# Kernel tuning notes

Measured on AMD Instinct MI355X. Metric: run time of the kernel, lower is better.

The kernel has to match this reference:

```python
import jax, jax.numpy as jnp
import numpy as np

N, E, IN, H, L = 50000, 640000, 64, 128, 3
EPS_DIST = 1e-8
LN_EPS = 1e-5


def setup_inputs() -> dict:
    key = jax.random.key(0)
    ks = iter(jax.random.split(key, 64))

    def rn(shape, fan_in):
        return (jax.random.normal(next(ks), shape, jnp.float32) / np.sqrt(fan_in)).astype(jnp.float32)

    inp = {}
    inp['h'] = jax.random.normal(next(ks), (N, IN), jnp.float32)
    inp['x'] = jax.random.normal(next(ks), (N, 3), jnp.float32)
    inp['edge_index'] = jax.random.randint(next(ks), (2, E), 0, N, jnp.int64)
    # embedding_in: Linear(IN, H)
    inp['W_emb'] = rn((IN, H), IN); inp['b_emb'] = jnp.zeros((H,), jnp.float32)
    # per-layer EquivariantConv params, stacked over L
    inp['Wm1'] = rn((L, 2 * H + 1, H), 2 * H + 1); inp['bm1'] = jnp.zeros((L, H), jnp.float32)
    inp['Wm2'] = rn((L, H, H), H);                 inp['bm2'] = jnp.zeros((L, H), jnp.float32)
    inp['Wc1'] = rn((L, H, H), H);                 inp['bc1'] = jnp.zeros((L, H), jnp.float32)
    inp['Wc2'] = rn((L, H, 1), H)  # no bias
    inp['Wn1'] = rn((L, 2 * H, H), 2 * H);         inp['bn1'] = jnp.zeros((L, H), jnp.float32)
    inp['Wn2'] = rn((L, H, H), H);                 inp['bn2'] = jnp.zeros((L, H), jnp.float32)
    inp['ln_g'] = jnp.ones((L, H), jnp.float32);   inp['ln_b'] = jnp.zeros((L, H), jnp.float32)
    # epsilon head params
    inp['Wem1'] = rn((2 * H + 4, H), 2 * H + 4);   inp['bem1'] = jnp.zeros((H,), jnp.float32)
    inp['Wem2'] = rn((H, H), H);                   inp['bem2'] = jnp.zeros((H,), jnp.float32)
    inp['Wec1'] = rn((H, H), H);                   inp['bec1'] = jnp.zeros((H,), jnp.float32)
    inp['Wec2'] = rn((H, 3), H);                   inp['bec2'] = jnp.zeros((3,), jnp.float32)
    inp['Wh1'] = rn((H + 3, H), H + 3);            inp['bh1'] = jnp.zeros((H,), jnp.float32)
    inp['Wh2'] = rn((H, 3), H);                    inp['bh2'] = jnp.zeros((3,), jnp.float32)
    return inp


def _layernorm(v, g, b):
    mu = jnp.mean(v, axis=-1, keepdims=True)
    var = jnp.mean((v - mu) ** 2, axis=-1, keepdims=True)
    return (v - mu) * jax.lax.rsqrt(var + LN_EPS) * g + b


def reference(h, x, edge_index, W_emb, b_emb, Wm1, bm1, Wm2, bm2, Wc1, bc1, Wc2,
              Wn1, bn1, Wn2, bn2, ln_g, ln_b, Wem1, bem1, Wem2, bem2,
              Wec1, bec1, Wec2, bec2, Wh1, bh1, Wh2, bh2):
    row, col = edge_index[0], edge_index[1]
    n = x.shape[0]
    seg = lambda v: jax.ops.segment_sum(v, col, num_segments=n)
    in_degree = seg(jnp.ones((col.shape[0], 1), x.dtype))  # [N,1]

    h = h @ W_emb + b_emb  # embedding_in

    for i in range(L):
        rel = x[row] - x[col]                                   # [E,3]
        dist = jnp.linalg.norm(rel, axis=-1, keepdims=True)     # [E,1]
        mi = jnp.concatenate([h[row], h[col], dist], axis=-1)   # [E,2H+1]
        m = jax.nn.silu(jax.nn.silu(mi @ Wm1[i] + bm1[i]) @ Wm2[i] + bm2[i])
        agg = seg(m)                                            # [N,H]
        rel_dir = rel / (dist + EPS_DIST)
        coord_mult = jnp.tanh(jax.nn.silu(m @ Wc1[i] + bc1[i]) @ Wc2[i])  # [E,1]
        coord_update = seg(coord_mult * rel_dir)                # [N,3]
        x = x + coord_update / (in_degree + 1.0)
        nu = jnp.concatenate([h, agg], axis=-1)
        h = h + jax.nn.silu(nu @ Wn1[i] + bn1[i]) @ Wn2[i] + bn2[i]
        h = _layernorm(h, ln_g[i], ln_b[i])

    # predict_epsilon (eps_directional_head=False, eps_use_local_head=True, eps_normalize_agg=False)
    rel = x[row] - x[col]
    dist = jnp.linalg.norm(rel, axis=-1, keepdims=True)
    mi = jnp.concatenate([h[row], h[col], rel, dist], axis=-1)  # [E,2H+4]
    em = jax.nn.silu(jax.nn.silu(mi @ Wem1 + bem1) @ Wem2 + bem2)
    eps_src = jax.nn.silu(em @ Wec1 + bec1) @ Wec2 + bec2       # [E,3]
    eps = seg(eps_src)                                          # [N,3]
    hx = jnp.concatenate([h, x], axis=-1)
    eps = eps + jax.nn.silu(hx @ Wh1 + bh1) @ Wh2 + bh2
    return (h, x, eps)
```

## Files before the change

### kernel.cpp

```cpp
#include <hip/hip_runtime.h>

#define N_NODES 50000
#define N_EDGES 640000
#define HDIM    128
#define NLAYERS 3

typedef __attribute__((ext_vector_type(4))) float f32x4;
typedef short s16x8 __attribute__((ext_vector_type(8)));
typedef __bf16 bf16v8 __attribute__((ext_vector_type(8)));

static __device__ __forceinline__ unsigned short f2b(float f){
  unsigned int u = __float_as_uint(f);
  unsigned int r = u + 0x7FFFu + ((u >> 16) & 1u);
  return (unsigned short)(r >> 16);
}
static __device__ __forceinline__ float b2f(unsigned short h){
  return __uint_as_float(((unsigned int)h) << 16);
}
static __device__ __forceinline__ float silu_f(float x){
  return x / (1.0f + __expf(-x));
}
static __device__ __forceinline__ unsigned int cvt2(float a, float b){
  unsigned int r;
  asm("v_cvt_pk_bf16_f32 %0, %1, %2" : "=v"(r) : "v"(a), "v"(b));
  return r;
}
static __device__ __forceinline__ s16x8 siluPack(const f32x4 a, const f32x4 b){
  union { unsigned int u[4]; s16x8 v; } r;
  r.u[0] = cvt2(silu_f(a[0]), silu_f(a[1]));
  r.u[1] = cvt2(silu_f(a[2]), silu_f(a[3]));
  r.u[2] = cvt2(silu_f(b[0]), silu_f(b[1]));
  r.u[3] = cvt2(silu_f(b[2]), silu_f(b[3]));
  return r.v;
}
static __device__ __forceinline__ f32x4 MFMA(s16x8 a, s16x8 b, f32x4 c){
  return __builtin_amdgcn_mfma_f32_16x16x32_bf16(
      __builtin_bit_cast(bf16v8, a), __builtin_bit_cast(bf16v8, b), c, 0, 0, 0);
}

static __device__ __forceinline__ s16x8 ldA(const unsigned short* __restrict__ WT,
                                            int K, int s, int kk, int lane){
  const unsigned short* p = WT + (size_t)((s<<4) + (lane&15))*K + (kk<<5) + ((lane>>4)<<2);
  ushort4 a = *(const ushort4*)p;
  ushort4 b = *(const ushort4*)(p + 16);
  s16x8 r;
  r[0]=(short)a.x; r[1]=(short)a.y; r[2]=(short)a.z; r[3]=(short)a.w;
  r[4]=(short)b.x; r[5]=(short)b.y; r[6]=(short)b.z; r[7]=(short)b.w;
  return r;
}
static __device__ __forceinline__ s16x8 ldBf32(const float* __restrict__ p, int q){
  float4 a = *(const float4*)(p + (q<<2));
  float4 b = *(const float4*)(p + 16 + (q<<2));
  s16x8 r;
  r[0]=(short)f2b(a.x); r[1]=(short)f2b(a.y); r[2]=(short)f2b(a.z); r[3]=(short)f2b(a.w);
  r[4]=(short)f2b(b.x); r[5]=(short)f2b(b.y); r[6]=(short)f2b(b.z); r[7]=(short)f2b(b.w);
  return r;
}

#define GLL(SRC, DST) __builtin_amdgcn_global_load_lds( \
    (const __attribute__((address_space(1))) void*)(SRC), \
    (__attribute__((address_space(3))) void*)(DST), 16, 0, 0)

static __device__ __forceinline__ void segAtomicAdd(float* addr_base, int key,
                                                    float v, int lane, int q){
  #pragma unroll
  for (int d=1; d<16; d<<=1){
    const float ov = __shfl_up(v, d);
    const int  ok = __shfl_up(key, d);
    if ((lane&15) >= d && ok == key) v += ov;
  }
  const int nk = __shfl_down(key, 1);
  const bool last = ((lane&15)==15) || (nk != key);
  if (last) atomicAdd(addr_base + (size_t)key*3 + q, v);
}

struct ConvJob { const float* src; unsigned short* dst; int kshift; };
struct ConvJobs { ConvJob j[8]; };
__global__ void k_conv8(ConvJobs jobs){
  const ConvJob jb = jobs.j[blockIdx.y];
  const int K = 1 << jb.kshift;
  const int idx = (blockIdx.x<<8) + threadIdx.x;
  if (idx < (K<<7)){
    const int n = idx >> jb.kshift;
    const int k = idx & (K-1);
    jb.dst[idx] = f2b(jb.src[(size_t)k*HDIM + n]);
  }
}

struct BlobJob { const float *W1, *W2, *W3; unsigned short* dst; };
struct BlobJobs { BlobJob j[4]; };
__global__ void k_blob4(BlobJobs jobs){
  const BlobJob jb = jobs.j[blockIdx.y];
  const int i = (blockIdx.x<<8) + threadIdx.x;
  const int t = i >> 12;
  const int n = (i >> 5) & 127;
  const int slot = (i >> 3) & 3;
  const int j = i & 7;
  const int q = slot ^ ((n >> 1) & 3);
  const int kl = ((j >> 2) << 4) + (q << 2) + (j & 3);
  float v;
  if (t < 8)       v = jb.W1[(size_t)((t<<5)+kl)*HDIM + n];
  else if (t < 12) v = jb.W2[(size_t)(((t-8)<<5)+kl)*HDIM + n];
  else             v = jb.W3[(size_t)(((t-12)<<5)+kl)*HDIM + n];
  jb.dst[i] = f2b(v);
}

__global__ void k_init(const float* __restrict__ xin, float* __restrict__ xbuf,
                       float* __restrict__ cu, float* __restrict__ epsb,
                       int* __restrict__ degi){
  const int i = (blockIdx.x<<8) + threadIdx.x;
  if (i < N_NODES*3){ xbuf[i] = xin[i]; cu[i] = 0.f; epsb[i] = 0.f; }
  if (i < N_NODES) degi[i] = 0;
}

__global__ void k_degree(const int* __restrict__ coli, int* __restrict__ degi){
  const int e = (blockIdx.x<<8) + threadIdx.x;
  if (e < N_EDGES) atomicAdd(&degi[coli[e]], 1);
}
__global__ void k_scanA(const int* __restrict__ degi, int* __restrict__ off, int* __restrict__ bsum){
  const int t = threadIdx.x, b = blockIdx.x;
  const int i = (b<<8) + t;
  const int v = (i < N_NODES) ? degi[i] : 0;
  int x = v;
  const int lane = t & 63;
  #pragma unroll
  for (int d=1; d<64; d<<=1){ int y = __shfl_up(x, d); if (lane >= d) x += y; }
  __shared__ int wsum[4];
  if (lane == 63) wsum[t>>6] = x;
  __syncthreads();
  int wo = 0;
  #pragma unroll
  for (int w=0; w<4; ++w) if (w < (t>>6)) wo += wsum[w];
  const int incl = x + wo;
  if (i < N_NODES) off[i] = incl - v;
  if (t == 255) bsum[b] = incl;
}
__global__ void k_scanB(int* __restrict__ bsum, int nb){
  const int t = threadIdx.x;
  const int v = (t < nb) ? bsum[t] : 0;
  int x = v;
  const int lane = t & 63;
  #pragma unroll
  for (int d=1; d<64; d<<=1){ int y = __shfl_up(x, d); if (lane >= d) x += y; }
  __shared__ int wsum[4];
  if (lane == 63) wsum[t>>6] = x;
  __syncthreads();
  int wo = 0;
  #pragma unroll
  for (int w=0; w<4; ++w) if (w < (t>>6)) wo += wsum[w];
  const int incl = x + wo;
  if (t < nb) bsum[t] = incl - v;
}
__global__ void k_scanC(int* __restrict__ off, const int* __restrict__ bsum, int* __restrict__ cursor){
  const int i = (blockIdx.x<<8) + threadIdx.x;
  if (i < N_NODES){
    const int o = off[i] + bsum[i>>8];
    off[i] = o;
    cursor[i] = o;
  }
}
__global__ void k_fill(const int* __restrict__ rowi, const int* __restrict__ coli,
                       int* __restrict__ cursor,
                       int* __restrict__ rowS, int* __restrict__ colS){
  const int e = (blockIdx.x<<8) + threadIdx.x;
  if (e < N_EDGES){
    const int c = coli[e];
    const int p = atomicAdd(&cursor[c], 1);
    rowS[p] = rowi[e];
    colS[p] = c;
  }
}

__global__ __launch_bounds__(256) void k_embed(
    const float* __restrict__ hin, const unsigned short* __restrict__ WembT,
    const float* __restrict__ bemb, float* __restrict__ hbuf,
    unsigned short* __restrict__ hb)
{
  __shared__ float s_b[128];
  const int tid = threadIdx.x;
  if (tid < 128) s_b[tid] = bemb[tid];
  __syncthreads();
  const int lane = tid & 63, q = lane>>4;
  const int n = (blockIdx.x<<6) + ((tid>>6)<<4) + (lane&15);
  const bool valid = n < N_NODES;
  const int nc = valid ? n : (N_NODES-1);
  const float* __restrict__ hp = hin + (size_t)nc*64;
  f32x4 acc[8];
  #pragma unroll
  for (int s=0;s<8;++s)
    #pragma unroll
    for (int r=0;r<4;++r) acc[s][r] = s_b[(s<<4)+(q<<2)+r];
  #pragma unroll
  for (int kk=0;kk<2;++kk){
    const s16x8 bf = ldBf32(hp + (kk<<5), q);
    #pragma unroll
    for (int s=0;s<8;++s) acc[s] = MFMA(ldA(WembT, 64, s, kk, lane), bf, acc[s]);
  }
  if (valid){
    float* op = hbuf + (size_t)n*HDIM;
    unsigned short* hbw = hb + (size_t)n*HDIM;
    #pragma unroll
    for (int s=0;s<8;++s){
      float4 o; o.x=acc[s][0]; o.y=acc[s][1]; o.z=acc[s][2]; o.w=acc[s][3];
      *(float4*)(op + (s<<4) + (q<<2)) = o;
      ushort4 u; u.x=f2b(o.x); u.y=f2b(o.y); u.z=f2b(o.z); u.w=f2b(o.w);
      *(ushort4*)(hbw + ((s>>1)<<5) + (q<<3) + ((s&1)<<2)) = u;
    }
  }
}

__global__ __launch_bounds__(1024,1) void k_edge_mlp(
    const unsigned short* __restrict__ hb, const float* __restrict__ xbuf,
    const int* __restrict__ rowS, const int* __restrict__ colS,
    const unsigned short* __restrict__ blob,
    const float* __restrict__ bm1v, const float* __restrict__ wm1r,
    const float* __restrict__ bm2v, const float* __restrict__ bc1v,
    const float* __restrict__ wc2v,
    unsigned short* __restrict__ m_buf, float* __restrict__ cu)
{
  __shared__ struct {
    __align__(16) unsigned char wbuf[16][8192];
    float rdS[3][512];
  } sm;
  const int tid = threadIdx.x, lane = tid & 63, q = lane >> 4;
  const int w = tid >> 6;
  const int q8 = q << 3;
  const int ebase = blockIdx.x << 9;

  {
    const unsigned short* bsrc = blob + (tid<<3);
    unsigned char* bdst = ((unsigned char*)sm.wbuf) + (tid<<4);
    #pragma unroll
    for (int i=0;i<8;++i)
      GLL(bsrc + (i<<13), bdst + (i<<14));
  }

  int rn[2], cn[2];
  float dist[2];
  #pragma unroll
  for (int e=0;e<2;++e){
    const int el = (w<<5) + (e<<4) + (lane&15);
    const int ge = ebase + el;
    rn[e] = rowS[ge]; cn[e] = colS[ge];
    const float dx = xbuf[3*rn[e]+0] - xbuf[3*cn[e]+0];
    const float dy = xbuf[3*rn[e]+1] - xbuf[3*cn[e]+1];
    const float dz = xbuf[3*rn[e]+2] - xbuf[3*cn[e]+2];
    const float d = sqrtf(dx*dx + dy*dy + dz*dz);
    dist[e] = d;
    if (q == 0){
      const float inv = 1.0f / (d + 1e-8f);
      sm.rdS[0][el] = dx*inv; sm.rdS[1][el] = dy*inv; sm.rdS[2][el] = dz*inv;
    }
  }

  f32x4 acc[2][8];
  #pragma unroll
  for (int s=0;s<8;++s){
    const f32x4 b1 = *(const f32x4*)&bm1v[(s<<4)+(q<<2)];
    const f32x4 wv = *(const f32x4*)&wm1r[(s<<4)+(q<<2)];
    #pragma unroll
    for (int e=0;e<2;++e)
      #pragma unroll
      for (int r=0;r<4;++r) acc[e][s][r] = b1[r] + dist[e]*wv[r];
  }
  const int toff = ((lane&15)<<6) + ((q ^ ((lane>>1)&3))<<4);

  s16x8 B0[2], B1[2];
  #pragma unroll
  for (int e=0;e<2;++e){
    B0[e] = *(const s16x8*)(hb + ((size_t)rn[e]<<7) + q8);
    B1[e] = *(const s16x8*)(hb + ((size_t)rn[e]<<7) + 32 + q8);
  }

  __syncthreads();

  #pragma unroll
  for (int kk=0;kk<8;++kk){
    s16x8 Bn[2];
    if (kk < 6){
      const int k2 = kk+2;
      #pragma unroll
      for (int e=0;e<2;++e){
        const int node = (k2 < 4) ? rn[e] : cn[e];
        Bn[e] = *(const s16x8*)(hb + ((size_t)node<<7) + ((k2&3)<<5) + q8);
      }
    }
    #pragma unroll
    for (int s=0;s<8;++s){
      const s16x8 A = *(const s16x8*)&sm.wbuf[kk][(s<<10)+toff];
      #pragma unroll
      for (int e=0;e<2;++e) acc[e][s] = MFMA(A, B0[e], acc[e][s]);
    }
    #pragma unroll
    for (int e=0;e<2;++e){ B0[e] = B1[e]; if (kk < 6) B1[e] = Bn[e]; }
  }

  s16x8 sb[2][4];
  #pragma unroll
  for (int e=0;e<2;++e)
    #pragma unroll
    for (int c=0;c<4;++c) sb[e][c] = siluPack(acc[e][2*c], acc[e][2*c+1]);

  f32x4 acc2[2][8];
  #pragma unroll
  for (int s=0;s<8;++s){
    const f32x4 b = *(const f32x4*)&bm2v[(s<<4)+(q<<2)];
    #pragma unroll
    for (int e=0;e<2;++e) acc2[e][s] = b;
  }
  #pragma unroll
  for (int c=0;c<4;++c)
    #pragma unroll
    for (int s=0;s<8;++s){
      const s16x8 A = *(const s16x8*)&sm.wbuf[8+c][(s<<10)+toff];
      #pragma unroll
      for (int e=0;e<2;++e) acc2[e][s] = MFMA(A, sb[e][c], acc2[e][s]);
    }

  s16x8 mb[2][4];
  #pragma unroll
  for (int e=0;e<2;++e)
    #pragma unroll
    for (int c=0;c<4;++c) mb[e][c] = siluPack(acc2[e][2*c], acc2[e][2*c+1]);

  f32x4 acc3[2][8];
  #pragma unroll
  for (int s=0;s<8;++s){
    const f32x4 b = *(const f32x4*)&bc1v[(s<<4)+(q<<2)];
    #pragma unroll
    for (int e=0;e<2;++e) acc3[e][s] = b;
  }
  #pragma unroll
  for (int c=0;c<4;++c)
    #pragma unroll
    for (int s=0;s<8;++s){
      const s16x8 A = *(const s16x8*)&sm.wbuf[12+c][(s<<10)+toff];
      #pragma unroll
      for (int e=0;e<2;++e) acc3[e][s] = MFMA(A, mb[e][c], acc3[e][s]);
    }

  float dot[2] = {0.f,0.f};
  #pragma unroll
  for (int s=0;s<8;++s){
    const f32x4 wv = *(const f32x4*)&wc2v[(s<<4)+(q<<2)];
    #pragma unroll
    for (int e=0;e<2;++e)
      #pragma unroll
      for (int r=0;r<4;++r) dot[e] += silu_f(acc3[e][s][r]) * wv[r];
  }
  #pragma unroll
  for (int e=0;e<2;++e){
    dot[e] += __shfl_xor(dot[e], 16);
    dot[e] += __shfl_xor(dot[e], 32);
    const float cm = tanhf(dot[e]);
    const int el = (w<<5) + (e<<4) + (lane&15);
    if (q < 3)
      segAtomicAdd(cu, cn[e], cm * sm.rdS[q][el], lane, q);
  }
  #pragma unroll
  for (int e=0;e<2;++e){
    const int ge = ebase + (w<<5) + (e<<4) + (lane&15);
    unsigned short* mp = m_buf + ((size_t)ge<<7) + q8;
    #pragma unroll
    for (int c=0;c<4;++c) *(s16x8*)(mp + (c<<5)) = mb[e][c];
  }
}

__global__ __launch_bounds__(256) void k_node_mlp(
    float* __restrict__ hbuf, unsigned short* __restrict__ hb,
    float* __restrict__ xbuf,
    const unsigned short* __restrict__ m_buf,
    const int* __restrict__ off, const int* __restrict__ degi,
    float* __restrict__ cu,
    const unsigned short* __restrict__ Wn1T, const float* __restrict__ bn1v,
    const unsigned short* __restrict__ Wn2T, const float* __restrict__ bn2v,
    const float* __restrict__ lng, const float* __restrict__ lnb)
{
  __shared__ float s_bn1[128], s_bn2[128], s_g[128], s_b[128];
  const int tid = threadIdx.x;
  const int nbase = blockIdx.x << 6;
  if (tid >= 128){
    const int f = tid - 128;
    s_bn1[f]=bn1v[f]; s_bn2[f]=bn2v[f]; s_g[f]=lng[f]; s_b[f]=lnb[f];
  } else if (tid < 64){
    const int n = nbase + tid;
    if (n < N_NODES){
      const float dd = (float)degi[n] + 1.0f;
      #pragma unroll
      for (int c=0;c<3;++c){
        xbuf[3*n+c] += cu[3*n+c] / dd;
        cu[3*n+c] = 0.f;
      }
    }
  }
  __syncthreads();

  const int lane = tid & 63, q = lane >> 4;
  const int q8 = q << 3;
  const int n = nbase + ((tid>>6)<<4) + (lane & 15);
  const bool valid = (n < N_NODES);
  const int nc = valid ? n : (N_NODES-1);
  const float* __restrict__ hp = hbuf + (size_t)nc*HDIM;
  const unsigned short* __restrict__ hbp = hb + (size_t)nc*HDIM;

  float aggv[4][8];
  #pragma unroll
  for (int kk=0;kk<4;++kk)
    #pragma unroll
    for (int j=0;j<8;++j) aggv[kk][j]=0.f;
  {
    const int st = off[nc];
    const int cnt = degi[nc];
    for (int ii=0; ii<cnt; ++ii){
      const unsigned short* mrow = m_buf + ((size_t)(st+ii)<<7);
      #pragma unroll
      for (int kk=0;kk<4;++kk){
        const s16x8 v = *(const s16x8*)(mrow + (kk<<5) + q8);
        #pragma unroll
        for (int j=0;j<8;++j) aggv[kk][j] += b2f((unsigned short)v[j]);
      }
    }
  }

  f32x4 acc[8];
  #pragma unroll
  for (int s=0;s<8;++s)
    #pragma unroll
    for (int r=0;r<4;++r) acc[s][r] = s_bn1[(s<<4)+(q<<2)+r];
  #pragma unroll
  for (int kk=0;kk<4;++kk){
    const s16x8 bf = *(const s16x8*)(hbp + (kk<<5) + q8);
    #pragma unroll
    for (int s=0;s<8;++s) acc[s] = MFMA(ldA(Wn1T, 256, s, kk, lane), bf, acc[s]);
  }
  #pragma unroll
  for (int kk=0;kk<4;++kk){
    s16x8 bf;
    #pragma unroll
    for (int j=0;j<8;++j) bf[j] = (short)f2b(aggv[kk][j]);
    #pragma unroll
    for (int s=0;s<8;++s) acc[s] = MFMA(ldA(Wn1T, 256, s, kk+4, lane), bf, acc[s]);
  }
  s16x8 sb[4];
  #pragma unroll
  for (int t=0;t<4;++t)
    #pragma unroll
    for (int j=0;j<8;++j)
      sb[t][j] = (short)f2b(silu_f(acc[(t<<1)+(j>>2)][j&3]));
  f32x4 acc2[8];
  #pragma unroll
  for (int s=0;s<8;++s)
    #pragma unroll
    for (int r=0;r<4;++r) acc2[s][r] = s_bn2[(s<<4)+(q<<2)+r];
  #pragma unroll
  for (int kk=0;kk<4;++kk){
    #pragma unroll
    for (int s=0;s<8;++s) acc2[s] = MFMA(ldA(Wn2T, 128, s, kk, lane), sb[kk], acc2[s]);
  }

  float v[8][4];
  float sum = 0.f;
  #pragma unroll
  for (int s=0;s<8;++s){
    float4 h4 = *(const float4*)(hp + (s<<4) + (q<<2));
    v[s][0] = h4.x + acc2[s][0]; v[s][1] = h4.y + acc2[s][1];
    v[s][2] = h4.z + acc2[s][2]; v[s][3] = h4.w + acc2[s][3];
    sum += v[s][0]+v[s][1]+v[s][2]+v[s][3];
  }
  sum += __shfl_xor(sum, 16);
  sum += __shfl_xor(sum, 32);
  const float mu = sum * (1.0f/128.0f);
  float vs = 0.f;
  #pragma unroll
  for (int s=0;s<8;++s)
    #pragma unroll
    for (int r=0;r<4;++r){ const float d = v[s][r]-mu; vs += d*d; }
  vs += __shfl_xor(vs, 16);
  vs += __shfl_xor(vs, 32);
  const float rs = rsqrtf(vs*(1.0f/128.0f) + 1e-5f);
  if (valid){
    float* op = hbuf + (size_t)n*HDIM;
    unsigned short* hbw = hb + (size_t)n*HDIM;
    #pragma unroll
    for (int s=0;s<8;++s){
      const int f0 = (s<<4)+(q<<2);
      float4 o;
      o.x = (v[s][0]-mu)*rs*s_g[f0+0] + s_b[f0+0];
      o.y = (v[s][1]-mu)*rs*s_g[f0+1] + s_b[f0+1];
      o.z = (v[s][2]-mu)*rs*s_g[f0+2] + s_b[f0+2];
      o.w = (v[s][3]-mu)*rs*s_g[f0+3] + s_b[f0+3];
      *(float4*)(op + f0) = o;
      ushort4 u; u.x=f2b(o.x); u.y=f2b(o.y); u.z=f2b(o.z); u.w=f2b(o.w);
      *(ushort4*)(hbw + ((s>>1)<<5) + q8 + ((s&1)<<2)) = u;
    }
  }
}

__global__ __launch_bounds__(1024,1) void k_eps_edge(
    const unsigned short* __restrict__ hb, const float* __restrict__ xbuf,
    const int* __restrict__ rowS, const int* __restrict__ colS,
    const unsigned short* __restrict__ blob,
    const float* __restrict__ bem1v, const float* __restrict__ wem_rows,
    const float* __restrict__ bem2v, const float* __restrict__ bec1v,
    const float* __restrict__ Wec2, const float* __restrict__ bec2,
    float* __restrict__ epsb)
{
  __shared__ struct {
    __align__(16) unsigned char wbuf[16][8192];
    float wcs[3][128];
  } sm;
  const int tid = threadIdx.x, lane = tid & 63, q = lane >> 4;
  const int w = tid >> 6;
  const int q8 = q << 3;
  const int ebase = blockIdx.x << 9;

  {
    const unsigned short* bsrc = blob + (tid<<3);
    unsigned char* bdst = ((unsigned char*)sm.wbuf) + (tid<<4);
    #pragma unroll
    for (int i=0;i<8;++i)
      GLL(bsrc + (i<<13), bdst + (i<<14));
  }
  if (tid < 128){
    sm.wcs[0][tid] = Wec2[tid*3+0];
    sm.wcs[1][tid] = Wec2[tid*3+1];
    sm.wcs[2][tid] = Wec2[tid*3+2];
  }

  int rn[2], cn[2];
  float rl0[2], rl1[2], rl2[2], dist[2];
  #pragma unroll
  for (int e=0;e<2;++e){
    const int ge = ebase + (w<<5) + (e<<4) + (lane&15);
    rn[e] = rowS[ge]; cn[e] = colS[ge];
    const float dx = xbuf[3*rn[e]+0] - xbuf[3*cn[e]+0];
    const float dy = xbuf[3*rn[e]+1] - xbuf[3*cn[e]+1];
    const float dz = xbuf[3*rn[e]+2] - xbuf[3*cn[e]+2];
    rl0[e]=dx; rl1[e]=dy; rl2[e]=dz;
    dist[e] = sqrtf(dx*dx + dy*dy + dz*dz);
  }

  f32x4 acc[2][8];
  #pragma unroll
  for (int s=0;s<8;++s){
    const int f4 = (s<<4)+(q<<2);
    const f32x4 b1 = *(const f32x4*)&bem1v[f4];
    const f32x4 w0 = *(const f32x4*)&wem_rows[f4];
    const f32x4 w1 = *(const f32x4*)&wem_rows[128+f4];
    const f32x4 w2 = *(const f32x4*)&wem_rows[256+f4];
    const f32x4 w3 = *(const f32x4*)&wem_rows[384+f4];
    #pragma unroll
    for (int e=0;e<2;++e)
      #pragma unroll
      for (int r=0;r<4;++r)
        acc[e][s][r] = b1[r] + rl0[e]*w0[r] + rl1[e]*w1[r] + rl2[e]*w2[r] + dist[e]*w3[r];
  }
  const int toff = ((lane&15)<<6) + ((q ^ ((lane>>1)&3))<<4);

  s16x8 B0[2], B1[2];
  #pragma unroll
  for (int e=0;e<2;++e){
    B0[e] = *(const s16x8*)(hb + ((size_t)rn[e]<<7) + q8);
    B1[e] = *(const s16x8*)(hb + ((size_t)rn[e]<<7) + 32 + q8);
  }

  __syncthreads();

  #pragma unroll
  for (int kk=0;kk<8;++kk){
    s16x8 Bn[2];
    if (kk < 6){
      const int k2 = kk+2;
      #pragma unroll
      for (int e=0;e<2;++e){
        const int node = (k2 < 4) ? rn[e] : cn[e];
        Bn[e] = *(const s16x8*)(hb + ((size_t)node<<7) + ((k2&3)<<5) + q8);
      }
    }
    #pragma unroll
    for (int s=0;s<8;++s){
      const s16x8 A = *(const s16x8*)&sm.wbuf[kk][(s<<10)+toff];
      #pragma unroll
      for (int e=0;e<2;++e) acc[e][s] = MFMA(A, B0[e], acc[e][s]);
    }
    #pragma unroll
    for (int e=0;e<2;++e){ B0[e] = B1[e]; if (kk < 6) B1[e] = Bn[e]; }
  }

  s16x8 sb[2][4];
  #pragma unroll
  for (int e=0;e<2;++e)
    #pragma unroll
    for (int c=0;c<4;++c) sb[e][c] = siluPack(acc[e][2*c], acc[e][2*c+1]);

  f32x4 acc2[2][8];
  #pragma unroll
  for (int s=0;s<8;++s){
    const f32x4 b = *(const f32x4*)&bem2v[(s<<4)+(q<<2)];
    #pragma unroll
    for (int e=0;e<2;++e) acc2[e][s] = b;
  }
  #pragma unroll
  for (int c=0;c<4;++c)
    #pragma unroll
    for (int s=0;s<8;++s){
      const s16x8 A = *(const s16x8*)&sm.wbuf[8+c][(s<<10)+toff];
      #pragma unroll
      for (int e=0;e<2;++e) acc2[e][s] = MFMA(A, sb[e][c], acc2[e][s]);
    }

  s16x8 mb[2][4];
  #pragma unroll
  for (int e=0;e<2;++e)
    #pragma unroll
    for (int c=0;c<4;++c) mb[e][c] = siluPack(acc2[e][2*c], acc2[e][2*c+1]);

  f32x4 acc3[2][8];
  #pragma unroll
  for (int s=0;s<8;++s){
    const f32x4 b = *(const f32x4*)&bec1v[(s<<4)+(q<<2)];
    #pragma unroll
    for (int e=0;e<2;++e) acc3[e][s] = b;
  }
  #pragma unroll
  for (int c=0;c<4;++c)
    #pragma unroll
    for (int s=0;s<8;++s){
      const s16x8 A = *(const s16x8*)&sm.wbuf[12+c][(s<<10)+toff];
      #pragma unroll
      for (int e=0;e<2;++e) acc3[e][s] = MFMA(A, mb[e][c], acc3[e][s]);
    }

  float d0[2]={0,0}, d1[2]={0,0}, d2[2]={0,0};
  #pragma unroll
  for (int s=0;s<8;++s){
    const int f4 = (s<<4)+(q<<2);
    const f32x4 w0 = *(const f32x4*)&sm.wcs[0][f4];
    const f32x4 w1 = *(const f32x4*)&sm.wcs[1][f4];
    const f32x4 w2 = *(const f32x4*)&sm.wcs[2][f4];
    #pragma unroll
    for (int e=0;e<2;++e)
      #pragma unroll
      for (int r=0;r<4;++r){
        const float ev = silu_f(acc3[e][s][r]);
        d0[e] += ev*w0[r]; d1[e] += ev*w1[r]; d2[e] += ev*w2[r];
      }
  }
  #pragma unroll
  for (int e=0;e<2;++e){
    d0[e] += __shfl_xor(d0[e],16); d0[e] += __shfl_xor(d0[e],32);
    d1[e] += __shfl_xor(d1[e],16); d1[e] += __shfl_xor(d1[e],32);
    d2[e] += __shfl_xor(d2[e],16); d2[e] += __shfl_xor(d2[e],32);
    if (q < 3){
      const float val = ((q==0)?d0[e]:((q==1)?d1[e]:d2[e])) + bec2[q];
      segAtomicAdd(epsb, cn[e], val, lane, q);
    }
  }
}

__global__ __launch_bounds__(256) void k_eps_node(
    const float* __restrict__ hbuf, const float* __restrict__ xbuf,
    const unsigned short* __restrict__ Wh1T, const float* __restrict__ bh1v,
    const float* __restrict__ wh1_rows,
    const float* __restrict__ Wh2, const float* __restrict__ bh2,
    float* __restrict__ epsb)
{
  __shared__ float s_bh1[128], s_w3[3][128], s_wc[3][128];
  const int tid = threadIdx.x;
  if (tid >= 128){
    const int f = tid - 128;
    s_bh1[f]=bh1v[f];
    s_w3[0][f]=wh1_rows[f]; s_w3[1][f]=wh1_rows[128+f]; s_w3[2][f]=wh1_rows[256+f];
    s_wc[0][f]=Wh2[f*3+0]; s_wc[1][f]=Wh2[f*3+1]; s_wc[2][f]=Wh2[f*3+2];
  }
  __syncthreads();
  const int lane = tid & 63, q = lane >> 4;
  const int n = (blockIdx.x<<6) + ((tid>>6)<<4) + (lane & 15);
  const bool valid = n < N_NODES;
  const int nc = valid ? n : (N_NODES-1);
  const float* __restrict__ hp = hbuf + (size_t)nc*HDIM;
  const float x0 = xbuf[3*nc+0], x1 = xbuf[3*nc+1], x2 = xbuf[3*nc+2];
  f32x4 acc[8];
  #pragma unroll
  for (int s=0;s<8;++s)
    #pragma unroll
    for (int r=0;r<4;++r){
      const int f = (s<<4)+(q<<2)+r;
      acc[s][r] = s_bh1[f] + x0*s_w3[0][f] + x1*s_w3[1][f] + x2*s_w3[2][f];
    }
  #pragma unroll
  for (int kk=0;kk<4;++kk){
    const s16x8 bf = ldBf32(hp + (kk<<5), q);
    #pragma unroll
    for (int s=0;s<8;++s) acc[s] = MFMA(ldA(Wh1T, 128, s, kk, lane), bf, acc[s]);
  }
  float d0=0.f, d1=0.f, d2=0.f;
  #pragma unroll
  for (int s=0;s<8;++s)
    #pragma unroll
    for (int r=0;r<4;++r){
      const int f = (s<<4)+(q<<2)+r;
      const float ev = silu_f(acc[s][r]);
      d0 += ev*s_wc[0][f]; d1 += ev*s_wc[1][f]; d2 += ev*s_wc[2][f];
    }
  d0 += __shfl_xor(d0,16); d0 += __shfl_xor(d0,32);
  d1 += __shfl_xor(d1,16); d1 += __shfl_xor(d1,32);
  d2 += __shfl_xor(d2,16); d2 += __shfl_xor(d2,32);
  if (valid && q < 3){
    const float val = (q==0)?d0:((q==1)?d1:d2);
    epsb[(size_t)n*3 + q] += val + bh2[q];
  }
}

extern "C" void kernel_launch(void* const* d_in, const int* in_sizes, int n_in,
                              void* d_out, int out_size, void* d_ws, size_t ws_size,
                              hipStream_t stream)
{
  (void)in_sizes; (void)n_in; (void)out_size; (void)ws_size;
  const float* h_in  = (const float*)d_in[0];
  const float* x_in  = (const float*)d_in[1];
  const int*   eidx  = (const int*)d_in[2];
  const float* W_emb = (const float*)d_in[3];
  const float* b_emb = (const float*)d_in[4];
  const float* Wm1 = (const float*)d_in[5];
  const float* bm1 = (const float*)d_in[6];
  const float* Wm2 = (const float*)d_in[7];
  const float* bm2 = (const float*)d_in[8];
  const float* Wc1 = (const float*)d_in[9];
  const float* bc1 = (const float*)d_in[10];
  const float* Wc2 = (const float*)d_in[11];
  const float* Wn1 = (const float*)d_in[12];
  const float* bn1 = (const float*)d_in[13];
  const float* Wn2 = (const float*)d_in[14];
  const float* bn2 = (const float*)d_in[15];
  const float* lng = (const float*)d_in[16];
  const float* lnb = (const float*)d_in[17];
  const float* Wem1 = (const float*)d_in[18];
  const float* bem1 = (const float*)d_in[19];
  const float* Wem2 = (const float*)d_in[20];
  const float* bem2 = (const float*)d_in[21];
  const float* Wec1 = (const float*)d_in[22];
  const float* bec1 = (const float*)d_in[23];
  const float* Wec2 = (const float*)d_in[24];
  const float* bec2 = (const float*)d_in[25];
  const float* Wh1 = (const float*)d_in[26];
  const float* bh1 = (const float*)d_in[27];
  const float* Wh2 = (const float*)d_in[28];
  const float* bh2 = (const float*)d_in[29];

  const int* rowi = eidx;
  const int* coli = eidx + N_EDGES;

  float* hbuf = (float*)d_out;
  float* xbuf = hbuf + (size_t)N_NODES*HDIM;
  float* epsb = xbuf + (size_t)N_NODES*3;

  char* wp = (char*)d_ws;
  auto alloc = [&](size_t bytes)->char*{
    char* p = wp; wp += (bytes + 255) & ~(size_t)255; return p;
  };
  unsigned short* WembT = (unsigned short*)alloc((size_t)128*64*2);
  unsigned short *Wn1T[NLAYERS], *Wn2T[NLAYERS];
  for (int i=0;i<NLAYERS;++i){
    Wn1T[i] = (unsigned short*)alloc((size_t)128*256*2);
    Wn2T[i] = (unsigned short*)alloc((size_t)128*128*2);
  }
  unsigned short* Wh1T  = (unsigned short*)alloc((size_t)128*128*2);
  unsigned short* blobL = (unsigned short*)alloc((size_t)NLAYERS*16*4096*2);
  unsigned short* blobE = (unsigned short*)alloc((size_t)16*4096*2);
  unsigned short* hb    = (unsigned short*)alloc((size_t)N_NODES*HDIM*2);
  int* degi   = (int*)alloc((size_t)N_NODES*4);
  int* offv   = (int*)alloc((size_t)N_NODES*4);
  int* cursor = (int*)alloc((size_t)N_NODES*4);
  int* bsum   = (int*)alloc(4096);
  float* cu   = (float*)alloc((size_t)N_NODES*3*4);
  int* rowS   = (int*)alloc((size_t)N_EDGES*4);
  int* colS   = (int*)alloc((size_t)N_EDGES*4);
  unsigned short* m_buf = (unsigned short*)alloc((size_t)N_EDGES*HDIM*2);

  ConvJobs cj;
  cj.j[0] = {W_emb, WembT, 6};
  for (int i=0;i<NLAYERS;++i){
    cj.j[1+i] = {Wn1 + (size_t)i*256*128, Wn1T[i], 8};
    cj.j[4+i] = {Wn2 + (size_t)i*128*128, Wn2T[i], 7};
  }
  cj.j[7] = {Wh1, Wh1T, 7};
  k_conv8<<<dim3(128,8), dim3(256), 0, stream>>>(cj);

  BlobJobs bj;
  for (int i=0;i<NLAYERS;++i)
    bj.j[i] = {Wm1 + (size_t)i*257*128, Wm2 + (size_t)i*128*128,
               Wc1 + (size_t)i*128*128, blobL + (size_t)i*16*4096};
  bj.j[3] = {Wem1, Wem2, Wec1, blobE};
  k_blob4<<<dim3(256,4), dim3(256), 0, stream>>>(bj);

  k_init<<<dim3((N_NODES*3+255)/256), dim3(256), 0, stream>>>(x_in, xbuf, cu, epsb, degi);

  k_degree<<<dim3((N_EDGES+255)/256), dim3(256), 0, stream>>>(coli, degi);
  const int nb = (N_NODES + 255)/256;
  k_scanA<<<dim3(nb), dim3(256), 0, stream>>>(degi, offv, bsum);
  k_scanB<<<dim3(1), dim3(256), 0, stream>>>(bsum, nb);
  k_scanC<<<dim3(nb), dim3(256), 0, stream>>>(offv, bsum, cursor);
  k_fill<<<dim3((N_EDGES+255)/256), dim3(256), 0, stream>>>(rowi, coli, cursor, rowS, colS);

  k_embed<<<dim3((N_NODES+63)/64), dim3(256), 0, stream>>>(h_in, WembT, b_emb, hbuf, hb);

  for (int i=0;i<NLAYERS;++i){
    const unsigned short* blob_i = blobL + (size_t)i*16*4096;
    const float* wm1r = Wm1 + (size_t)i*257*128 + (size_t)256*128;
    k_edge_mlp<<<dim3(N_EDGES/512), dim3(1024), 0, stream>>>(
      hb, xbuf, rowS, colS, blob_i,
      bm1 + i*128, wm1r, bm2 + i*128, bc1 + i*128, Wc2 + i*128,
      m_buf, cu);
    k_node_mlp<<<dim3((N_NODES+63)/64), dim3(256), 0, stream>>>(
      hbuf, hb, xbuf, m_buf, offv, degi, cu,
      Wn1T[i], bn1 + i*128, Wn2T[i], bn2 + i*128, lng + i*128, lnb + i*128);
  }
  k_eps_edge<<<dim3(N_EDGES/512), dim3(1024), 0, stream>>>(
    hb, xbuf, rowS, colS, blobE,
    bem1, Wem1 + (size_t)256*128, bem2, bec1, Wec2, bec2, epsb);
  k_eps_node<<<dim3((N_NODES+63)/64), dim3(256), 0, stream>>>(
    hbuf, xbuf, Wh1T, bh1, Wh1 + (size_t)128*128, Wh2, bh2, epsb);
}
```

Measured before the change: 1.373 ms.

## Stream edge-MLP weights through double-buffered LDS with smaller blocks and more edges per wave

The edge MLP kernels previously loaded all 128KB of bf16 weights into LDS up front, using 1024-thread blocks at one block per CU. They now use 256-thread blocks that double-buffer 32KB weight slices with async global-to-LDS loads, aiming for two or more resident blocks per CU. Each wave now handles 64 edges instead of 32, so every weight read from LDS feeds more MFMAs. Weight loads overlap with compute, at the cost of more barriers, more weight reloads across blocks, and higher register pressure. silu and tanh also switch to raw v_rcp-based forms.

```diff
diff --git a/kernel.cpp b/kernel.cpp
--- a/kernel.cpp
+++ b/kernel.cpp
@@ -17,8 +17,14 @@
 static __device__ __forceinline__ float b2f(unsigned short h){
   return __uint_as_float(((unsigned int)h) << 16);
 }
+static __device__ __forceinline__ float rcp_f(float x){
+  float r; asm("v_rcp_f32 %0, %1" : "=v"(r) : "v"(x)); return r;
+}
 static __device__ __forceinline__ float silu_f(float x){
-  return x / (1.0f + __expf(-x));
+  return x * rcp_f(1.0f + __expf(-x));
+}
+static __device__ __forceinline__ float tanh_f(float x){
+  return 1.0f - 2.0f * rcp_f(__expf(2.0f*x) + 1.0f);
 }
 static __device__ __forceinline__ unsigned int cvt2(float a, float b){
   unsigned int r;
@@ -60,6 +66,15 @@
 #define GLL(SRC, DST) __builtin_amdgcn_global_load_lds( \
     (const __attribute__((address_space(1))) void*)(SRC), \
     (__attribute__((address_space(3))) void*)(DST), 16, 0, 0)
+
+#define STG2(T0,BUF) do{ \
+    const unsigned short* _s = blob + (((size_t)(T0))<<12) + (tid<<3); \
+    unsigned char* _d = &sm.wbuf[BUF][tid<<4]; \
+    GLL(_s, _d); GLL(_s+2048, _d+4096); GLL(_s+4096, _d+8192); GLL(_s+6144, _d+12288); \
+  }while(0)
+#define WAITV(N) asm volatile("s_waitcnt vmcnt(" #N ")" ::: "memory")
+#define BARF do{ __builtin_amdgcn_s_barrier(); asm volatile("" ::: "memory"); }while(0)
+#define EBAR do{ asm volatile("" ::: "memory"); __builtin_amdgcn_s_barrier(); }while(0)
 
 static __device__ __forceinline__ void segAtomicAdd(float* addr_base, int key,
                                                     float v, int lane, int q){
@@ -209,7 +224,7 @@
   }
 }
 
-__global__ __launch_bounds__(1024,1) void k_edge_mlp(
+__global__ __launch_bounds__(256,2) void k_edge_mlp(
     const unsigned short* __restrict__ hb, const float* __restrict__ xbuf,
     const int* __restrict__ rowS, const int* __restrict__ colS,
     const unsigned short* __restrict__ blob,
@@ -219,27 +234,21 @@
     unsigned short* __restrict__ m_buf, float* __restrict__ cu)
 {
   __shared__ struct {
-    __align__(16) unsigned char wbuf[16][8192];
-    float rdS[3][512];
+    __align__(16) unsigned char wbuf[2][16384];
+    float rdS[3][256];
   } sm;
   const int tid = threadIdx.x, lane = tid & 63, q = lane >> 4;
   const int w = tid >> 6;
   const int q8 = q << 3;
-  const int ebase = blockIdx.x << 9;
-
-  {
-    const unsigned short* bsrc = blob + (tid<<3);
-    unsigned char* bdst = ((unsigned char*)sm.wbuf) + (tid<<4);
-    #pragma unroll
-    for (int i=0;i<8;++i)
-      GLL(bsrc + (i<<13), bdst + (i<<14));
-  }
-
-  int rn[2], cn[2];
-  float dist[2];
-  #pragma unroll
-  for (int e=0;e<2;++e){
-    const int el = (w<<5) + (e<<4) + (lane&15);
+  const int ebase = blockIdx.x << 8;
+
+  STG2(0,0); STG2(2,1);
+
+  int rn[4], cn[4];
+  float dist[4];
+  #pragma unroll
+  for (int e=0;e<4;++e){
+    const int el = (w<<6) + (e<<4) + (lane&15);
     const int ge = ebase + el;
     rn[e] = rowS[ge]; cn[e] = colS[ge];
     const float dx = xbuf[3*rn[e]+0] - xbuf[3*cn[e]+0];
@@ -248,118 +257,136 @@
     const float d = sqrtf(dx*dx + dy*dy + dz*dz);
     dist[e] = d;
     if (q == 0){
-      const float inv = 1.0f / (d + 1e-8f);
+      const float inv = rcp_f(d + 1e-8f);
       sm.rdS[0][el] = dx*inv; sm.rdS[1][el] = dy*inv; sm.rdS[2][el] = dz*inv;
     }
   }
 
-  f32x4 acc[2][8];
+  f32x4 acc[4][8];
   #pragma unroll
   for (int s=0;s<8;++s){
     const f32x4 b1 = *(const f32x4*)&bm1v[(s<<4)+(q<<2)];
     const f32x4 wv = *(const f32x4*)&wm1r[(s<<4)+(q<<2)];
     #pragma unroll
-    for (int e=0;e<2;++e)
+    for (int e=0;e<4;++e)
       #pragma unroll
       for (int r=0;r<4;++r) acc[e][s][r] = b1[r] + dist[e]*wv[r];
   }
   const int toff = ((lane&15)<<6) + ((q ^ ((lane>>1)&3))<<4);
 
-  s16x8 B0[2], B1[2];
-  #pragma unroll
-  for (int e=0;e<2;++e){
-    B0[e] = *(const s16x8*)(hb + ((size_t)rn[e]<<7) + q8);
-    B1[e] = *(const s16x8*)(hb + ((size_t)rn[e]<<7) + 32 + q8);
-  }
-
-  __syncthreads();
-
-  #pragma unroll
-  for (int kk=0;kk<8;++kk){
-    s16x8 Bn[2];
-    if (kk < 6){
-      const int k2 = kk+2;
-      #pragma unroll
-      for (int e=0;e<2;++e){
-        const int node = (k2 < 4) ? rn[e] : cn[e];
-        Bn[e] = *(const s16x8*)(hb + ((size_t)node<<7) + ((k2&3)<<5) + q8);
-      }
-    }
-    #pragma unroll
-    for (int s=0;s<8;++s){
-      const s16x8 A = *(const s16x8*)&sm.wbuf[kk][(s<<10)+toff];
-      #pragma unroll
-      for (int e=0;e<2;++e) acc[e][s] = MFMA(A, B0[e], acc[e][s]);
-    }
-    #pragma unroll
-    for (int e=0;e<2;++e){ B0[e] = B1[e]; if (kk < 6) B1[e] = Bn[e]; }
-  }
-
-  s16x8 sb[2][4];
-  #pragma unroll
-  for (int e=0;e<2;++e)
+  s16x8 Bc[4][2], Bn[4][2];
+  #pragma unroll
+  for (int e=0;e<4;++e){
+    Bc[e][0] = *(const s16x8*)(hb + ((size_t)rn[e]<<7) + q8);
+    Bc[e][1] = *(const s16x8*)(hb + ((size_t)rn[e]<<7) + 32 + q8);
+  }
+
+  #pragma unroll
+  for (int p=0;p<4;++p){
+    WAITV(4); BARF;
+    if (p < 3){
+      #pragma unroll
+      for (int e=0;e<4;++e){
+        const int kkA = 2*p+2, kkB = 2*p+3;
+        const unsigned short* nA = hb + ((size_t)((kkA<4)?rn[e]:cn[e])<<7) + ((kkA&3)<<5) + q8;
+        const unsigned short* nB = hb + ((size_t)((kkB<4)?rn[e]:cn[e])<<7) + ((kkB&3)<<5) + q8;
+        Bn[e][0] = *(const s16x8*)nA;
+        Bn[e][1] = *(const s16x8*)nB;
+      }
+    }
+    #pragma unroll
+    for (int t=0;t<2;++t)
+      #pragma unroll
+      for (int s=0;s<8;++s){
+        const s16x8 A = *(const s16x8*)&sm.wbuf[p&1][(t<<13)+(s<<10)+toff];
+        #pragma unroll
+        for (int e=0;e<4;++e) acc[e][s] = MFMA(A, Bc[e][t], acc[e][s]);
+      }
+    EBAR;
+    STG2(4+2*p, p&1);
+    if (p < 3){
+      #pragma unroll
+      for (int e=0;e<4;++e){ Bc[e][0]=Bn[e][0]; Bc[e][1]=Bn[e][1]; }
+    }
+  }
+
+  s16x8 sb[4][4];
+  #pragma unroll
+  for (int e=0;e<4;++e)
     #pragma unroll
     for (int c=0;c<4;++c) sb[e][c] = siluPack(acc[e][2*c], acc[e][2*c+1]);
 
-  f32x4 acc2[2][8];
+  f32x4 acc2[4][8];
   #pragma unroll
   for (int s=0;s<8;++s){
     const f32x4 b = *(const f32x4*)&bm2v[(s<<4)+(q<<2)];
     #pragma unroll
-    for (int e=0;e<2;++e) acc2[e][s] = b;
-  }
-  #pragma unroll
-  for (int c=0;c<4;++c)
-    #pragma unroll
-    for (int s=0;s<8;++s){
-      const s16x8 A = *(const s16x8*)&sm.wbuf[8+c][(s<<10)+toff];
-      #pragma unroll
-      for (int e=0;e<2;++e) acc2[e][s] = MFMA(A, sb[e][c], acc2[e][s]);
-    }
-
-  s16x8 mb[2][4];
-  #pragma unroll
-  for (int e=0;e<2;++e)
+    for (int e=0;e<4;++e) acc2[e][s] = b;
+  }
+  #pragma unroll
+  for (int p=0;p<2;++p){
+    WAITV(4); BARF;
+    #pragma unroll
+    for (int t=0;t<2;++t)
+      #pragma unroll
+      for (int s=0;s<8;++s){
+        const s16x8 A = *(const s16x8*)&sm.wbuf[p&1][(t<<13)+(s<<10)+toff];
+        #pragma unroll
+        for (int e=0;e<4;++e) acc2[e][s] = MFMA(A, sb[e][2*p+t], acc2[e][s]);
+      }
+    EBAR;
+    if (p == 0) STG2(12, 0); else STG2(14, 1);
+  }
+
+  s16x8 mb[4][4];
+  #pragma unroll
+  for (int e=0;e<4;++e)
     #pragma unroll
     for (int c=0;c<4;++c) mb[e][c] = siluPack(acc2[e][2*c], acc2[e][2*c+1]);
 
-  f32x4 acc3[2][8];
+  f32x4 acc3[4][8];
   #pragma unroll
   for (int s=0;s<8;++s){
     const f32x4 b = *(const f32x4*)&bc1v[(s<<4)+(q<<2)];
     #pragma unroll
-    for (int e=0;e<2;++e) acc3[e][s] = b;
-  }
-  #pragma unroll
-  for (int c=0;c<4;++c)
-    #pragma unroll
-    for (int s=0;s<8;++s){
-      const s16x8 A = *(const s16x8*)&sm.wbuf[12+c][(s<<10)+toff];
-      #pragma unroll
-      for (int e=0;e<2;++e) acc3[e][s] = MFMA(A, mb[e][c], acc3[e][s]);
-    }
-
-  float dot[2] = {0.f,0.f};
+    for (int e=0;e<4;++e) acc3[e][s] = b;
+  }
+  #pragma unroll
+  for (int p=0;p<2;++p){
+    if (p == 0){ WAITV(4); } else { WAITV(0); }
+    BARF;
+    #pragma unroll
+    for (int t=0;t<2;++t)
+      #pragma unroll
+      for (int s=0;s<8;++s){
+        const s16x8 A = *(const s16x8*)&sm.wbuf[p&1][(t<<13)+(s<<10)+toff];
+        #pragma unroll
+        for (int e=0;e<4;++e) acc3[e][s] = MFMA(A, mb[e][2*p+t], acc3[e][s]);
+      }
+    if (p == 0) EBAR;
+  }
+
+  float dot[4] = {0.f,0.f,0.f,0.f};
   #pragma unroll
   for (int s=0;s<8;++s){
     const f32x4 wv = *(const f32x4*)&wc2v[(s<<4)+(q<<2)];
     #pragma unroll
-    for (int e=0;e<2;++e)
+    for (int e=0;e<4;++e)
       #pragma unroll
       for (int r=0;r<4;++r) dot[e] += silu_f(acc3[e][s][r]) * wv[r];
   }
   #pragma unroll
-  for (int e=0;e<2;++e){
+  for (int e=0;e<4;++e){
     dot[e] += __shfl_xor(dot[e], 16);
     dot[e] += __shfl_xor(dot[e], 32);
-    const float cm = tanhf(dot[e]);
-    const int el = (w<<5) + (e<<4) + (lane&15);
+    const float cm = tanh_f(dot[e]);
+    const int el = (w<<6) + (e<<4) + (lane&15);
     if (q < 3)
       segAtomicAdd(cu, cn[e], cm * sm.rdS[q][el], lane, q);
   }
   #pragma unroll
-  for (int e=0;e<2;++e){
-    const int ge = ebase + (w<<5) + (e<<4) + (lane&15);
+  for (int e=0;e<4;++e){
+    const int ge = ebase + (w<<6) + (e<<4) + (lane&15);
     unsigned short* mp = m_buf + ((size_t)ge<<7) + q8;
     #pragma unroll
     for (int c=0;c<4;++c) *(s16x8*)(mp + (c<<5)) = mb[e][c];
@@ -496,7 +523,7 @@
   }
 }
 
-__global__ __launch_bounds__(1024,1) void k_eps_edge(
+__global__ __launch_bounds__(256,2) void k_eps_edge(
     const unsigned short* __restrict__ hb, const float* __restrict__ xbuf,
     const int* __restrict__ rowS, const int* __restrict__ colS,
     const unsigned short* __restrict__ blob,
@@ -506,32 +533,26 @@
     float* __restrict__ epsb)
 {
   __shared__ struct {
-    __align__(16) unsigned char wbuf[16][8192];
+    __align__(16) unsigned char wbuf[2][16384];
     float wcs[3][128];
   } sm;
   const int tid = threadIdx.x, lane = tid & 63, q = lane >> 4;
   const int w = tid >> 6;
   const int q8 = q << 3;
-  const int ebase = blockIdx.x << 9;
-
-  {
-    const unsigned short* bsrc = blob + (tid<<3);
-    unsigned char* bdst = ((unsigned char*)sm.wbuf) + (tid<<4);
-    #pragma unroll
-    for (int i=0;i<8;++i)
-      GLL(bsrc + (i<<13), bdst + (i<<14));
-  }
+  const int ebase = blockIdx.x << 8;
+
+  STG2(0,0); STG2(2,1);
   if (tid < 128){
     sm.wcs[0][tid] = Wec2[tid*3+0];
     sm.wcs[1][tid] = Wec2[tid*3+1];
     sm.wcs[2][tid] = Wec2[tid*3+2];
   }
 
-  int rn[2], cn[2];
-  float rl0[2], rl1[2], rl2[2], dist[2];
-  #pragma unroll
-  for (int e=0;e<2;++e){
-    const int ge = ebase + (w<<5) + (e<<4) + (lane&15);
+  int rn[4], cn[4];
+  float rl0[4], rl1[4], rl2[4], dist[4];
+  #pragma unroll
+  for (int e=0;e<4;++e){
+    const int ge = ebase + (w<<6) + (e<<4) + (lane&15);
     rn[e] = rowS[ge]; cn[e] = colS[ge];
     const float dx = xbuf[3*rn[e]+0] - xbuf[3*cn[e]+0];
     const float dy = xbuf[3*rn[e]+1] - xbuf[3*cn[e]+1];
@@ -540,7 +561,7 @@
     dist[e] = sqrtf(dx*dx + dy*dy + dz*dz);
   }
 
-  f32x4 acc[2][8];
+  f32x4 acc[4][8];
   #pragma unroll
   for (int s=0;s<8;++s){
     const int f4 = (s<<4)+(q<<2);
@@ -550,88 +571,106 @@
     const f32x4 w2 = *(const f32x4*)&wem_rows[256+f4];
     const f32x4 w3 = *(const f32x4*)&wem_rows[384+f4];
     #pragma unroll
-    for (int e=0;e<2;++e)
+    for (int e=0;e<4;++e)
       #pragma unroll
       for (int r=0;r<4;++r)
         acc[e][s][r] = b1[r] + rl0[e]*w0[r] + rl1[e]*w1[r] + rl2[e]*w2[r] + dist[e]*w3[r];
   }
   const int toff = ((lane&15)<<6) + ((q ^ ((lane>>1)&3))<<4);
 
-  s16x8 B0[2], B1[2];
-  #pragma unroll
-  for (int e=0;e<2;++e){
-    B0[e] = *(const s16x8*)(hb + ((size_t)rn[e]<<7) + q8);
-    B1[e] = *(const s16x8*)(hb + ((size_t)rn[e]<<7) + 32 + q8);
-  }
-
-  __syncthreads();
-
-  #pragma unroll
-  for (int kk=0;kk<8;++kk){
-    s16x8 Bn[2];
-    if (kk < 6){
-      const int k2 = kk+2;
-      #pragma unroll
-      for (int e=0;e<2;++e){
-        const int node = (k2 < 4) ? rn[e] : cn[e];
-        Bn[e] = *(const s16x8*)(hb + ((size_t)node<<7) + ((k2&3)<<5) + q8);
-      }
-    }
-    #pragma unroll
-    for (int s=0;s<8;++s){
-      const s16x8 A = *(const s16x8*)&sm.wbuf[kk][(s<<10)+toff];
-      #pragma unroll
-      for (int e=0;e<2;++e) acc[e][s] = MFMA(A, B0[e], acc[e][s]);
-    }
-    #pragma unroll
-    for (int e=0;e<2;++e){ B0[e] = B1[e]; if (kk < 6) B1[e] = Bn[e]; }
-  }
-
-  s16x8 sb[2][4];
-  #pragma unroll
-  for (int e=0;e<2;++e)
+  s16x8 Bc[4][2], Bn[4][2];
+  #pragma unroll
+  for (int e=0;e<4;++e){
+    Bc[e][0] = *(const s16x8*)(hb + ((size_t)rn[e]<<7) + q8);
+    Bc[e][1] = *(const s16x8*)(hb + ((size_t)rn[e]<<7) + 32 + q8);
+  }
+
+  #pragma unroll
+  for (int p=0;p<4;++p){
+    WAITV(4); BARF;
+    if (p < 3){
+      #pragma unroll
+      for (int e=0;e<4;++e){
+        const int kkA = 2*p+2, kkB = 2*p+3;
+        const unsigned short* nA = hb + ((size_t)((kkA<4)?rn[e]:cn[e])<<7) + ((kkA&3)<<5) + q8;
+        const unsigned short* nB = hb + ((size_t)((kkB<4)?rn[e]:cn[e])<<7) + ((kkB&3)<<5) + q8;
+        Bn[e][0] = *(const s16x8*)nA;
+        Bn[e][1] = *(const s16x8*)nB;
+      }
+    }
+    #pragma unroll
+    for (int t=0;t<2;++t)
+      #pragma unroll
+      for (int s=0;s<8;++s){
+        const s16x8 A = *(const s16x8*)&sm.wbuf[p&1][(t<<13)+(s<<10)+toff];
+        #pragma unroll
+        for (int e=0;e<4;++e) acc[e][s] = MFMA(A, Bc[e][t], acc[e][s]);
+      }
+    EBAR;
+    STG2(4+2*p, p&1);
+    if (p < 3){
+      #pragma unroll
+      for (int e=0;e<4;++e){ Bc[e][0]=Bn[e][0]; Bc[e][1]=Bn[e][1]; }
+    }
+  }
+
+  s16x8 sb[4][4];
+  #pragma unroll
+  for (int e=0;e<4;++e)
     #pragma unroll
     for (int c=0;c<4;++c) sb[e][c] = siluPack(acc[e][2*c], acc[e][2*c+1]);
 
-  f32x4 acc2[2][8];
+  f32x4 acc2[4][8];
   #pragma unroll
   for (int s=0;s<8;++s){
     const f32x4 b = *(const f32x4*)&bem2v[(s<<4)+(q<<2)];
     #pragma unroll
-    for (int e=0;e<2;++e) acc2[e][s] = b;
-  }
-  #pragma unroll
-  for (int c=0;c<4;++c)
-    #pragma unroll
-    for (int s=0;s<8;++s){
-      const s16x8 A = *(const s16x8*)&sm.wbuf[8+c][(s<<10)+toff];
-      #pragma unroll
-      for (int e=0;e<2;++e) acc2[e][s] = MFMA(A, sb[e][c], acc2[e][s]);
-    }
-
-  s16x8 mb[2][4];
-  #pragma unroll
-  for (int e=0;e<2;++e)
+    for (int e=0;e<4;++e) acc2[e][s] = b;
+  }
+  #pragma unroll
+  for (int p=0;p<2;++p){
+    WAITV(4); BARF;
+    #pragma unroll
+    for (int t=0;t<2;++t)
+      #pragma unroll
+      for (int s=0;s<8;++s){
+        const s16x8 A = *(const s16x8*)&sm.wbuf[p&1][(t<<13)+(s<<10)+toff];
+        #pragma unroll
+        for (int e=0;e<4;++e) acc2[e][s] = MFMA(A, sb[e][2*p+t], acc2[e][s]);
+      }
+    EBAR;
+    if (p == 0) STG2(12, 0); else STG2(14, 1);
+  }
+
+  s16x8 mb[4][4];
+  #pragma unroll
+  for (int e=0;e<4;++e)
     #pragma unroll
     for (int c=0;c<4;++c) mb[e][c] = siluPack(acc2[e][2*c], acc2[e][2*c+1]);
 
-  f32x4 acc3[2][8];
+  f32x4 acc3[4][8];
   #pragma unroll
   for (int s=0;s<8;++s){
     const f32x4 b = *(const f32x4*)&bec1v[(s<<4)+(q<<2)];
     #pragma unroll
-    for (int e=0;e<2;++e) acc3[e][s] = b;
-  }
-  #pragma unroll
-  for (int c=0;c<4;++c)
-    #pragma unroll
-    for (int s=0;s<8;++s){
-      const s16x8 A = *(const s16x8*)&sm.wbuf[12+c][(s<<10)+toff];
-      #pragma unroll
-      for (int e=0;e<2;++e) acc3[e][s] = MFMA(A, mb[e][c], acc3[e][s]);
-    }
-
-  float d0[2]={0,0}, d1[2]={0,0}, d2[2]={0,0};
+    for (int e=0;e<4;++e) acc3[e][s] = b;
+  }
+  #pragma unroll
+  for (int p=0;p<2;++p){
+    if (p == 0){ WAITV(4); } else { WAITV(0); }
+    BARF;
+    #pragma unroll
+    for (int t=0;t<2;++t)
+      #pragma unroll
+      for (int s=0;s<8;++s){
+        const s16x8 A = *(const s16x8*)&sm.wbuf[p&1][(t<<13)+(s<<10)+toff];
+        #pragma unroll
+        for (int e=0;e<4;++e) acc3[e][s] = MFMA(A, mb[e][2*p+t], acc3[e][s]);
+      }
+    if (p == 0) EBAR;
+  }
+
+  float d0[4]={0,0,0,0}, d1[4]={0,0,0,0}, d2[4]={0,0,0,0};
   #pragma unroll
   for (int s=0;s<8;++s){
     const int f4 = (s<<4)+(q<<2);
@@ -639,7 +678,7 @@
     const f32x4 w1 = *(const f32x4*)&sm.wcs[1][f4];
     const f32x4 w2 = *(const f32x4*)&sm.wcs[2][f4];
     #pragma unroll
-    for (int e=0;e<2;++e)
+    for (int e=0;e<4;++e)
       #pragma unroll
       for (int r=0;r<4;++r){
         const float ev = silu_f(acc3[e][s][r]);
@@ -647,7 +686,7 @@
       }
   }
   #pragma unroll
-  for (int e=0;e<2;++e){
+  for (int e=0;e<4;++e){
     d0[e] += __shfl_xor(d0[e],16); d0[e] += __shfl_xor(d0[e],32);
     d1[e] += __shfl_xor(d1[e],16); d1[e] += __shfl_xor(d1[e],32);
     d2[e] += __shfl_xor(d2[e],16); d2[e] += __shfl_xor(d2[e],32);
@@ -808,7 +847,7 @@
   for (int i=0;i<NLAYERS;++i){
     const unsigned short* blob_i = blobL + (size_t)i*16*4096;
     const float* wm1r = Wm1 + (size_t)i*257*128 + (size_t)256*128;
-    k_edge_mlp<<<dim3(N_EDGES/512), dim3(1024), 0, stream>>>(
+    k_edge_mlp<<<dim3(N_EDGES/256), dim3(256), 0, stream>>>(
       hb, xbuf, rowS, colS, blob_i,
       bm1 + i*128, wm1r, bm2 + i*128, bc1 + i*128, Wc2 + i*128,
       m_buf, cu);
@@ -816,7 +855,7 @@
       hbuf, hb, xbuf, m_buf, offv, degi, cu,
       Wn1T[i], bn1 + i*128, Wn2T[i], bn2 + i*128, lng + i*128, lnb + i*128);
   }
-  k_eps_edge<<<dim3(N_EDGES/512), dim3(1024), 0, stream>>>(
+  k_eps_edge<<<dim3(N_EDGES/256), dim3(256), 0, stream>>>(
     hb, xbuf, rowS, colS, blobE,
     bem1, Wem1 + (size_t)256*128, bem2, bec1, Wec2, bec2, epsb);
   k_eps_node<<<dim3((N_NODES+63)/64), dim3(256), 0, stream>>>(
```

After: 1.415 ms. 3.0% more time.
